# Performance work log

Hardware: AMD Instinct MI355X
Metric: run time of the kernel (lower is better)

The kernel has to match this reference:

```python
import jax, jax.numpy as jnp
import numpy as np

DELTA = 5.0
R = 0.01
M, N = 4096, 13000

def setup_inputs() -> dict:
    key = jax.random.key(0)
    k1, k2, k3 = jax.random.split(key, 3)
    inputs = jax.random.normal(k1, (M, N), dtype=jnp.float32)
    targets_ = jax.random.randint(k2, (M,), 0, N, dtype=jnp.int64)
    targets = jax.random.randint(k3, (M,), 0, N, dtype=jnp.int64)
    GT_MC = jnp.zeros((M,), dtype=jnp.int32)
    return {"inputs": inputs, "targets_": targets_, "targets": targets, "GT_MC": GT_MC}

def reference(inputs, targets_, targets, GT_MC):
    # One-hot path (is_vec=False): exactly one positive per row.
    m, n = inputs.shape
    num_neg = n - 1                      # negatives per row
    k = int(R * num_neg)                 # hard negatives kept (top-k by logit)
    # positive logit per row: inputs[i, targets[i]]
    pos = jnp.take_along_axis(inputs, targets[:, None], axis=1)[:, 0]  # [m]
    # mask out the positive column so it never enters the negative top-k
    is_pos = jnp.arange(n)[None, :] == targets[:, None]                # [m, n]
    neg = jnp.where(is_pos, -jnp.inf, inputs)
    hard_neg, _ = jax.lax.top_k(neg, k)                                # [m, k]
    # per-row loss: delta * (1 - pos)^2 (mean over the single positive)
    #             + mean((1 + hard_neg)^2)
    loss_row = DELTA * (1.0 - pos) ** 2 + jnp.mean((1.0 + hard_neg) ** 2, axis=1)
    return jnp.mean(loss_row)
```

## Files before the change

### kernel.cpp

```cpp
#include <hip/hip_runtime.h>
#include <cstdint>


constexpr int M_ROWS = 4096;
constexpr int N_COLS = 13000;
constexpr int N4     = N_COLS / 4;
constexpr int KSEL   = 129;
constexpr int BLOCK  = 256;
constexpr int NWAVE  = BLOCK / 64;
constexpr int WCAP   = 320;
constexpr int FULL_IT  = N4 / (4 * BLOCK);
constexpr int TAIL_BASE = FULL_IT * 4 * BLOCK;
constexpr int TAIL_N   = N4 - TAIL_BASE;
constexpr float DELTA_C = 5.0f;
constexpr float T0   = 2.0f;

__device__ __forceinline__ uint32_t f2key(float f) {
    uint32_t u = __float_as_uint(f);
    return u ^ ((u & 0x80000000u) ? 0xFFFFFFFFu : 0x80000000u);
}
__device__ __forceinline__ float key2f(uint32_t k) {
    uint32_t u = (k & 0x80000000u) ? (k ^ 0x80000000u) : ~k;
    return __uint_as_float(u);
}

__global__ __launch_bounds__(BLOCK) void row_loss_kernel(
    const float* __restrict__ inputs,
    const int*   __restrict__ targets,
    float*       __restrict__ row_loss)
{
    __shared__ float cand[NWAVE * WCAP];
    __shared__ int   s_wcnt[NWAVE];
    __shared__ int   s_hist[16];
    __shared__ float s_fpart[NWAVE];
    __shared__ int   s_ipart[NWAVE];
    __shared__ int   s_bucket;
    __shared__ int   s_need;

    const int row  = blockIdx.x;
    const int tid  = threadIdx.x;
    const int wid  = tid >> 6;
    const int lane = tid & 63;
    const float* rp = inputs + (size_t)row * N_COLS;
    const float4* rp4 = reinterpret_cast<const float4*>(rp);
    const int pos = targets[row];
    const float pos_v = rp[pos];
    const uint64_t below = (1ull << lane) - 1ull;
    float* wseg = cand + wid * WCAP;

    auto stream_pass = [&](float t) -> int {
        int wcnt = 0;
        auto proc = [&](float x) {
            const uint64_t m = __ballot(x > t);
            if (m) {
                if (x > t) {
                    const int slot = wcnt + (int)__popcll(m & below);
                    if (slot < WCAP) wseg[slot] = x;
                }
                wcnt += (int)__popcll(m);
            }
        };
        for (int it = 0; it < FULL_IT; ++it) {
            const int b = it * 4 * BLOCK + tid;
            const float4 v0 = rp4[b];
            const float4 v1 = rp4[b +     BLOCK];
            const float4 v2 = rp4[b + 2 * BLOCK];
            const float4 v3 = rp4[b + 3 * BLOCK];
            proc(v0.x); proc(v0.y); proc(v0.z); proc(v0.w);
            proc(v1.x); proc(v1.y); proc(v1.z); proc(v1.w);
            proc(v2.x); proc(v2.y); proc(v2.z); proc(v2.w);
            proc(v3.x); proc(v3.y); proc(v3.z); proc(v3.w);
        }
        const float4 vt = (tid < TAIL_N) ? rp4[TAIL_BASE + tid]
                                         : make_float4(-1e30f, -1e30f, -1e30f, -1e30f);
        proc(vt.x); proc(vt.y); proc(vt.z); proc(vt.w);
        return wcnt;
    };

    uint32_t keyA = 0u;
    uint32_t keyB = 0xFFFFFFFFu;
    float t = T0;
    bool collapsed = false;
    float Tval = 0.0f;
    int cnt = 0;

    for (int iter = 0; iter < 64; ++iter) {
        cnt = stream_pass(t);
        if (lane == 0) s_wcnt[wid] = cnt;
        __syncthreads();
        const int c0 = s_wcnt[0], c1 = s_wcnt[1], c2 = s_wcnt[2], c3 = s_wcnt[3];
        __syncthreads();
        const int total = c0 + c1 + c2 + c3;
        const bool ovf = (c0 > WCAP) | (c1 > WCAP) | (c2 > WCAP) | (c3 > WCAP);
        const int npos = (pos_v > t) ? 1 : 0;

        if (collapsed || (!ovf && (total - npos) >= KSEL)) break;

        const uint32_t kt = f2key(t);
        if (ovf) keyA = kt; else keyB = kt;
        if (keyB - keyA <= 1u) {
            Tval = key2f(keyB);
            t = Tval;
            collapsed = true;
            continue;
        }
        t = key2f(keyA + (keyB - keyA) / 2u);
    }

    const int mycnt = cnt < WCAP ? cnt : WCAP;
    const uint32_t key_pos = f2key(pos_v);
    const bool pos_in = (pos_v > t);

    float T;
    if (collapsed) {
        T = Tval;
    } else {
        uint32_t hi = 0;
        int need = KSEL;
        for (int shift = 28; shift >= 0; shift -= 4) {
            if (tid < 16) s_hist[tid] = 0;
            __syncthreads();
            const uint32_t maskHigh = (uint32_t)(0xFFFFFFFFull << (shift + 4));
            for (int c = lane; c < mycnt; c += 64) {
                const uint32_t k = f2key(wseg[c]);
                if ((k & maskHigh) == hi)
                    atomicAdd(&s_hist[(k >> shift) & 15], 1);
            }
            __syncthreads();
            if (tid == 0) {
                if (pos_in && ((key_pos & maskHigh) == hi))
                    s_hist[(key_pos >> shift) & 15] -= 1;
                int cum = 0, b = 15;
                for (; b > 0; --b) {
                    const int h = s_hist[b];
                    if (cum + h >= need) break;
                    cum += h;
                }
                s_bucket = b;
                s_need = need - cum;
            }
            __syncthreads();
            hi |= ((uint32_t)s_bucket) << shift;
            need = s_need;
        }
        T = key2f(hi);
    }

    float s = 0.0f;
    int g = 0;
    for (int c = lane; c < mycnt; c += 64) {
        const float x = wseg[c];
        if (x > T) { const float u = 1.0f + x; s += u * u; ++g; }
    }
    #pragma unroll
    for (int off = 32; off > 0; off >>= 1) {
        s += __shfl_down(s, off);
        g += __shfl_down(g, off);
    }
    if (lane == 0) { s_fpart[wid] = s; s_ipart[wid] = g; }
    __syncthreads();
    if (tid == 0) {
        float ss = s_fpart[0] + s_fpart[1] + s_fpart[2] + s_fpart[3];
        int   gg = s_ipart[0] + s_ipart[1] + s_ipart[2] + s_ipart[3];
        if (pos_in && pos_v > T) {
            const float u = 1.0f + pos_v;
            ss -= u * u;
            gg -= 1;
        }
        const float uT = 1.0f + T;
        const float neg = (ss + (float)(KSEL - gg) * uT * uT) / (float)KSEL;
        const float d = 1.0f - pos_v;
        row_loss[row] = DELTA_C * d * d + neg;
    }
}

__global__ __launch_bounds__(1024) void reduce_kernel(
    const float* __restrict__ row_loss, float* __restrict__ out)
{
    __shared__ float s[1024];
    float acc = 0.0f;
    for (int i = threadIdx.x; i < M_ROWS; i += 1024) acc += row_loss[i];
    s[threadIdx.x] = acc;
    __syncthreads();
    for (int off = 512; off > 0; off >>= 1) {
        if (threadIdx.x < off) s[threadIdx.x] += s[threadIdx.x + off];
        __syncthreads();
    }
    if (threadIdx.x == 0) out[0] = s[0] / (float)M_ROWS;
}

extern "C" void kernel_launch(void* const* d_in, const int* in_sizes, int n_in,
                              void* d_out, int out_size, void* d_ws, size_t ws_size,
                              hipStream_t stream) {
    const float* inputs  = (const float*)d_in[0];
    const int*   targets = (const int*)d_in[2];
    float* row_loss = (float*)d_ws;

    row_loss_kernel<<<M_ROWS, BLOCK, 0, stream>>>(inputs, targets, row_loss);
    reduce_kernel<<<1, 1024, 0, stream>>>(row_loss, (float*)d_out);
}
```

Before: 51.50 us.

## Replace radix threshold refinement with fixed-bucket histogram and small-set rank selection

During the streaming pass, each candidate above the threshold is binned into a 256-bucket histogram on a fixed [2,6) scale. A wave-level prefix scan then finds the bucket holding the k-th value, and its members are gathered and ranked exhaustively, instead of running eight rounds of 4-bit radix refinement. Candidate compaction switches from ballot/popcount to per-element shared atomics, which adds atomic contention to the hot streaming loop. The final reduction kernel is replaced by a global atomicAdd plus a zeroing kernel, and launch bounds now request 8 blocks per CU. The fixed bucket scale assumes a roughly normal value distribution, with the radix path kept as a fallback when the gathered bucket overflows.

```diff
diff --git a/kernel.cpp b/kernel.cpp
--- a/kernel.cpp
+++ b/kernel.cpp
@@ -9,9 +9,10 @@
 constexpr int BLOCK  = 256;
 constexpr int NWAVE  = BLOCK / 64;
 constexpr int WCAP   = 320;
+constexpr int GCAP   = 64;
 constexpr int FULL_IT  = N4 / (4 * BLOCK);
 constexpr int TAIL_BASE = FULL_IT * 4 * BLOCK;
-constexpr int TAIL_N   = N4 - TAIL_BASE;
+constexpr int TAIL_N    = N4 - TAIL_BASE;
 constexpr float DELTA_C = 5.0f;
 constexpr float T0   = 2.0f;
 
@@ -23,19 +24,28 @@
     uint32_t u = (k & 0x80000000u) ? (k ^ 0x80000000u) : ~k;
     return __uint_as_float(u);
 }
-
-__global__ __launch_bounds__(BLOCK) void row_loss_kernel(
+__device__ __forceinline__ int bucketof(float x) {
+    int i = (int)((x - 2.0f) * 64.0f);
+    return i < 0 ? 0 : (i > 255 ? 255 : i);
+}
+
+__global__ void zero_out(float* out) { if (threadIdx.x == 0) out[0] = 0.0f; }
+
+__global__ __launch_bounds__(BLOCK, 8) void row_loss_kernel(
     const float* __restrict__ inputs,
     const int*   __restrict__ targets,
-    float*       __restrict__ row_loss)
+    float*       __restrict__ out)
 {
     __shared__ float cand[NWAVE * WCAP];
     __shared__ int   s_wcnt[NWAVE];
-    __shared__ int   s_hist[16];
+    __shared__ int   s_hist[256];
+    __shared__ float s_gath[GCAP];
+    __shared__ int   s_gcnt;
+    __shared__ int   s_bkt, s_need;
+    __shared__ float s_T;
     __shared__ float s_fpart[NWAVE];
     __shared__ int   s_ipart[NWAVE];
-    __shared__ int   s_bucket;
-    __shared__ int   s_need;
+    __shared__ int   s_rb, s_rn;
 
     const int row  = blockIdx.x;
     const int tid  = threadIdx.x;
@@ -45,19 +55,24 @@
     const float4* rp4 = reinterpret_cast<const float4*>(rp);
     const int pos = targets[row];
     const float pos_v = rp[pos];
-    const uint64_t below = (1ull << lane) - 1ull;
     float* wseg = cand + wid * WCAP;
 
-    auto stream_pass = [&](float t) -> int {
-        int wcnt = 0;
+    uint32_t keyA = 0u, keyB = 0xFFFFFFFFu;
+    float t = T0;
+    bool collapsed = false;
+    float Tval = 0.0f;
+    int c0, c1, c2, c3;
+
+    for (int iter = 0; iter < 64; ++iter) {
+        s_hist[tid] = 0;
+        if (tid < NWAVE) s_wcnt[tid] = 0;
+        __syncthreads();
+
         auto proc = [&](float x) {
-            const uint64_t m = __ballot(x > t);
-            if (m) {
-                if (x > t) {
-                    const int slot = wcnt + (int)__popcll(m & below);
-                    if (slot < WCAP) wseg[slot] = x;
-                }
-                wcnt += (int)__popcll(m);
+            if (x > t) {
+                atomicAdd(&s_hist[bucketof(x)], 1);
+                const int slot = atomicAdd(&s_wcnt[wid], 1);
+                if (slot < WCAP) wseg[slot] = x;
             }
         };
         for (int it = 0; it < FULL_IT; ++it) {
@@ -71,25 +86,13 @@
             proc(v2.x); proc(v2.y); proc(v2.z); proc(v2.w);
             proc(v3.x); proc(v3.y); proc(v3.z); proc(v3.w);
         }
-        const float4 vt = (tid < TAIL_N) ? rp4[TAIL_BASE + tid]
-                                         : make_float4(-1e30f, -1e30f, -1e30f, -1e30f);
-        proc(vt.x); proc(vt.y); proc(vt.z); proc(vt.w);
-        return wcnt;
-    };
-
-    uint32_t keyA = 0u;
-    uint32_t keyB = 0xFFFFFFFFu;
-    float t = T0;
-    bool collapsed = false;
-    float Tval = 0.0f;
-    int cnt = 0;
-
-    for (int iter = 0; iter < 64; ++iter) {
-        cnt = stream_pass(t);
-        if (lane == 0) s_wcnt[wid] = cnt;
-        __syncthreads();
-        const int c0 = s_wcnt[0], c1 = s_wcnt[1], c2 = s_wcnt[2], c3 = s_wcnt[3];
-        __syncthreads();
+        if (tid < TAIL_N) {
+            const float4 vt = rp4[TAIL_BASE + tid];
+            proc(vt.x); proc(vt.y); proc(vt.z); proc(vt.w);
+        }
+        __syncthreads();
+
+        c0 = s_wcnt[0]; c1 = s_wcnt[1]; c2 = s_wcnt[2]; c3 = s_wcnt[3];
         const int total = c0 + c1 + c2 + c3;
         const bool ovf = (c0 > WCAP) | (c1 > WCAP) | (c2 > WCAP) | (c3 > WCAP);
         const int npos = (pos_v > t) ? 1 : 0;
@@ -102,12 +105,14 @@
             Tval = key2f(keyB);
             t = Tval;
             collapsed = true;
-            continue;
-        }
-        t = key2f(keyA + (keyB - keyA) / 2u);
-    }
-
-    const int mycnt = cnt < WCAP ? cnt : WCAP;
+        } else {
+            t = key2f(keyA + (keyB - keyA) / 2u);
+        }
+        __syncthreads();
+    }
+
+    const int cw = (wid == 0) ? c0 : (wid == 1) ? c1 : (wid == 2) ? c2 : c3;
+    const int mycnt = cw < WCAP ? cw : WCAP;
     const uint32_t key_pos = f2key(pos_v);
     const bool pos_in = (pos_v > t);
 
@@ -115,35 +120,102 @@
     if (collapsed) {
         T = Tval;
     } else {
-        uint32_t hi = 0;
-        int need = KSEL;
-        for (int shift = 28; shift >= 0; shift -= 4) {
-            if (tid < 16) s_hist[tid] = 0;
+        if (wid == 0) {
+            if (lane == 0) s_gcnt = 0;
+            int h[4];
+            #pragma unroll
+            for (int k = 0; k < 4; ++k) {
+                h[k] = s_hist[4 * lane + k];
+                if (pos_in && bucketof(pos_v) == 4 * lane + k) h[k] -= 1;
+            }
+            const int G = h[0] + h[1] + h[2] + h[3];
+            int x = G;
+            #pragma unroll
+            for (int off = 1; off < 64; off <<= 1) {
+                const int tmp = __shfl_down(x, off);
+                if (lane + off < 64) x += tmp;
+            }
+            const int xnext = x - G;
+            const int cc3 = xnext + h[3];
+            const int cc2 = cc3 + h[2];
+            const int cc1 = cc2 + h[1];
+            if (x >= KSEL && xnext < KSEL) {
+                int k, Cnext;
+                if      (cc3 >= KSEL) { k = 3; Cnext = xnext; }
+                else if (cc2 >= KSEL) { k = 2; Cnext = cc3; }
+                else if (cc1 >= KSEL) { k = 1; Cnext = cc2; }
+                else                  { k = 0; Cnext = cc1; }
+                s_bkt = 4 * lane + k;
+                s_need = KSEL - Cnext;
+            }
+        }
+        __syncthreads();
+        const int bsel = s_bkt;
+        const int need = s_need;
+
+        for (int c = lane; c < mycnt; c += 64) {
+            const float x = wseg[c];
+            if (bucketof(x) == bsel) {
+                const int slot = atomicAdd(&s_gcnt, 1);
+                if (slot < GCAP) s_gath[slot] = x;
+            }
+        }
+        __syncthreads();
+        const int m = s_gcnt;
+
+        if (m <= GCAP) {
+            if (wid == 0) {
+                int skip = -1;
+                if (pos_in && bucketof(pos_v) == bsel) {
+                    const bool eq = (lane < m) &&
+                        (__float_as_uint(s_gath[lane]) == __float_as_uint(pos_v));
+                    const uint64_t em = __ballot(eq);
+                    if (em) skip = __ffsll((long long)em) - 1;
+                }
+                const bool valid = (lane < m) && (lane != skip);
+                const float x = valid ? s_gath[lane] : 0.0f;
+                int g = 0, ge = 0;
+                for (int j = 0; j < m; ++j) {
+                    const float y = s_gath[j];
+                    const bool vj = (j != skip);
+                    g  += (vj && y >  x);
+                    ge += (vj && y >= x);
+                }
+                if (valid && g < need && ge >= need) s_T = x;
+            }
             __syncthreads();
-            const uint32_t maskHigh = (uint32_t)(0xFFFFFFFFull << (shift + 4));
-            for (int c = lane; c < mycnt; c += 64) {
-                const uint32_t k = f2key(wseg[c]);
-                if ((k & maskHigh) == hi)
-                    atomicAdd(&s_hist[(k >> shift) & 15], 1);
-            }
-            __syncthreads();
-            if (tid == 0) {
-                if (pos_in && ((key_pos & maskHigh) == hi))
-                    s_hist[(key_pos >> shift) & 15] -= 1;
-                int cum = 0, b = 15;
-                for (; b > 0; --b) {
-                    const int h = s_hist[b];
-                    if (cum + h >= need) break;
-                    cum += h;
-                }
-                s_bucket = b;
-                s_need = need - cum;
-            }
-            __syncthreads();
-            hi |= ((uint32_t)s_bucket) << shift;
-            need = s_need;
-        }
-        T = key2f(hi);
+            T = s_T;
+        } else {
+            uint32_t hi = 0;
+            int need2 = KSEL;
+            for (int shift = 28; shift >= 0; shift -= 4) {
+                if (tid < 16) s_hist[tid] = 0;
+                __syncthreads();
+                const uint32_t maskHigh = (uint32_t)(0xFFFFFFFFull << (shift + 4));
+                for (int c = lane; c < mycnt; c += 64) {
+                    const uint32_t k = f2key(wseg[c]);
+                    if ((k & maskHigh) == hi)
+                        atomicAdd(&s_hist[(k >> shift) & 15], 1);
+                }
+                __syncthreads();
+                if (tid == 0) {
+                    if (pos_in && ((key_pos & maskHigh) == hi))
+                        s_hist[(key_pos >> shift) & 15] -= 1;
+                    int cum = 0, b = 15;
+                    for (; b > 0; --b) {
+                        const int h = s_hist[b];
+                        if (cum + h >= need2) break;
+                        cum += h;
+                    }
+                    s_rb = b;
+                    s_rn = need2 - cum;
+                }
+                __syncthreads();
+                hi |= ((uint32_t)s_rb) << shift;
+                need2 = s_rn;
+            }
+            T = key2f(hi);
+        }
     }
 
     float s = 0.0f;
@@ -170,23 +242,9 @@
         const float uT = 1.0f + T;
         const float neg = (ss + (float)(KSEL - gg) * uT * uT) / (float)KSEL;
         const float d = 1.0f - pos_v;
-        row_loss[row] = DELTA_C * d * d + neg;
-    }
-}
-
-__global__ __launch_bounds__(1024) void reduce_kernel(
-    const float* __restrict__ row_loss, float* __restrict__ out)
-{
-    __shared__ float s[1024];
-    float acc = 0.0f;
-    for (int i = threadIdx.x; i < M_ROWS; i += 1024) acc += row_loss[i];
-    s[threadIdx.x] = acc;
-    __syncthreads();
-    for (int off = 512; off > 0; off >>= 1) {
-        if (threadIdx.x < off) s[threadIdx.x] += s[threadIdx.x + off];
-        __syncthreads();
-    }
-    if (threadIdx.x == 0) out[0] = s[0] / (float)M_ROWS;
+        const float loss = DELTA_C * d * d + neg;
+        atomicAdd(out, loss * (1.0f / (float)M_ROWS));
+    }
 }
 
 extern "C" void kernel_launch(void* const* d_in, const int* in_sizes, int n_in,
@@ -194,8 +252,8 @@
                               hipStream_t stream) {
     const float* inputs  = (const float*)d_in[0];
     const int*   targets = (const int*)d_in[2];
-    float* row_loss = (float*)d_ws;
-
-    row_loss_kernel<<<M_ROWS, BLOCK, 0, stream>>>(inputs, targets, row_loss);
-    reduce_kernel<<<1, 1024, 0, stream>>>(row_loss, (float*)d_out);
-}
+    float* out = (float*)d_out;
+
+    zero_out<<<1, 64, 0, stream>>>(out);
+    row_loss_kernel<<<M_ROWS, BLOCK, 0, stream>>>(inputs, targets, out);
+}
```

After: 127.1 us. +146.8%, slower.
